# Optimization experiments

Measured on AMD Instinct MI355X. Metric: run time of the kernel, lower is better.

The kernel has to match this reference:

```python
import jax, jax.numpy as jnp
import numpy as np

DIM = 192
HEADS = 6
HD = DIM // HEADS
WS = 7
R = 128  # low-rank projected sequence length
N_FULL = 3136  # 56*56
B = 32


def setup_inputs() -> dict:
    key = jax.random.key(0)
    ks = jax.random.split(key, 9)
    s = 0.02
    return {
        "x": jax.random.normal(ks[0], (2048, WS * WS, DIM), dtype=jnp.float32),
        "qkv_w": jax.random.normal(ks[1], (3 * DIM, DIM), dtype=jnp.float32) * s,
        "qkv_b": jax.random.normal(ks[2], (3 * DIM,), dtype=jnp.float32) * s,
        "E_w": jax.random.normal(ks[3], (R, N_FULL), dtype=jnp.float32) * s,
        "E_b": jax.random.normal(ks[4], (R,), dtype=jnp.float32) * s,
        "F_w": jax.random.normal(ks[5], (R, N_FULL), dtype=jnp.float32) * s,
        "F_b": jax.random.normal(ks[6], (R,), dtype=jnp.float32) * s,
        "proj_w": jax.random.normal(ks[7], (DIM, DIM), dtype=jnp.float32) * s,
        "proj_b": jax.random.normal(ks[8], (DIM,), dtype=jnp.float32) * s,
        "h": 56,
        "w": 56,
    }


def reference(x, qkv_w, qkv_b, E_w, E_b, F_w, F_b, proj_w, proj_b, h, w):
    C = x.shape[-1]
    # window_reverse: (nW*B, ws*ws, C) -> (B, H*W, C)
    xw = x.reshape(-1, WS, WS, C)
    b = xw.shape[0] // ((h // WS) * (w // WS))
    xm = xw.reshape(b, h // WS, w // WS, WS, WS, C)
    xm = xm.transpose(0, 1, 3, 2, 4, 5).reshape(b, h * w, C)
    n = h * w
    scale = 1.0 / np.sqrt(HD)

    qkv = (xm @ qkv_w.T + qkv_b).reshape(b, n, 3, HEADS, HD)
    qkv = qkv.transpose(2, 0, 3, 1, 4)  # (3, b, heads, n, hd)
    q, k, v = qkv[0] * scale, qkv[1], qkv[2]

    # Linformer low-rank projection along sequence: (b,h,n,d) -> (b,h,R,d)
    k_low = jnp.einsum('bhnd,kn->bhkd', k, E_w) + E_b[None, None, :, None]
    v_low = jnp.einsum('bhnd,kn->bhkd', v, F_w) + F_b[None, None, :, None]

    attn = jnp.einsum('bhnd,bhkd->bhnk', q, k_low)  # (b, heads, n, R)
    attn = jax.nn.softmax(attn, axis=-1)

    out = jnp.einsum('bhnk,bhkd->bhnd', attn, v_low)
    out = out.transpose(0, 2, 1, 3).reshape(b, n, C)
    out = out @ proj_w.T + proj_b
    return out
```

## Files before the change

kernel.cpp:

```cpp
#include <hip/hip_runtime.h>

typedef __bf16 bf16;
typedef bf16 bf16x8 __attribute__((ext_vector_type(8)));
typedef bf16 bf16x4 __attribute__((ext_vector_type(4)));
typedef float f32x4 __attribute__((ext_vector_type(4)));

#define MFMA16(a,b,c) __builtin_amdgcn_mfma_f32_16x16x32_bf16(a,b,c,0,0,0)

#define NSEQ 3136
#define CDIM 192

__device__ inline bf16x8 cvt8(float4 a, float4 b) {
  bf16x8 r;
  r[0]=(bf16)a.x; r[1]=(bf16)a.y; r[2]=(bf16)a.z; r[3]=(bf16)a.w;
  r[4]=(bf16)b.x; r[5]=(bf16)b.y; r[6]=(bf16)b.z; r[7]=(bf16)b.w;
  return r;
}

__device__ inline bf16x4 cvt4(float4 a) {
  bf16x4 r;
  r[0]=(bf16)a.x; r[1]=(bf16)a.y; r[2]=(bf16)a.z; r[3]=(bf16)a.w;
  return r;
}

__global__ void k_convert(const float* __restrict__ qkv_w, const float* __restrict__ E_w,
                          const float* __restrict__ F_w, const float* __restrict__ proj_w,
                          bf16* __restrict__ qkvw, bf16* __restrict__ EF, bf16* __restrict__ projw) {
  int i4 = blockIdx.x * blockDim.x + threadIdx.x;
  const int tot4 = 950272 / 4;
  for (; i4 < tot4; i4 += gridDim.x * blockDim.x) {
    int i = i4 * 4;
    float4 f;
    bf16* dst;
    if (i < 110592)      { f = *(const float4*)(qkv_w + i);            dst = qkvw + i; }
    else if (i < 512000) { f = *(const float4*)(E_w + (i - 110592));   dst = EF + (i - 110592); }
    else if (i < 913408) { f = *(const float4*)(F_w + (i - 512000));   dst = EF + (i - 110592); }
    else                 { f = *(const float4*)(proj_w + (i - 913408)); dst = projw + (i - 913408); }
    *(bf16x4*)dst = cvt4(f);
  }
}

__global__ void k_rowsum(const float* __restrict__ E_w, const float* __restrict__ F_w,
                         float* __restrict__ rowsums) {
  __shared__ float red[4];
  int row = blockIdx.x;
  const float* src = (row < 128) ? (E_w + (long)row * NSEQ) : (F_w + (long)(row - 128) * NSEQ);
  float s = 0.f;
  for (int i = threadIdx.x; i < NSEQ; i += 256) s += src[i];
  for (int off = 32; off; off >>= 1) s += __shfl_xor(s, off);
  if ((threadIdx.x & 63) == 0) red[threadIdx.x >> 6] = s;
  __syncthreads();
  if (threadIdx.x == 0) rowsums[row] = red[0] + red[1] + red[2] + red[3];
}

__global__ void k_xT(const float* __restrict__ x, bf16* __restrict__ xmT) {
  __shared__ bf16 tile[64][196];
  int blk = blockIdx.x;
  int b = blk / 49, n0 = (blk % 49) * 64;
  int tid = threadIdx.x;
  for (int e = tid; e < 3072; e += 256) {
    int row = e / 48, c4 = e % 48;
    int n = n0 + row;
    int r = n / 56, cc = n % 56;
    long srcrow = (long)(b * 64 + (r / 7) * 8 + (cc / 7)) * 49 + (r % 7) * 7 + (cc % 7);
    float4 f = *(const float4*)(x + srcrow * 192 + c4 * 4);
    *(bf16x4*)&tile[row][c4 * 4] = cvt4(f);
  }
  __syncthreads();
  for (int e = tid; e < 1536; e += 256) {
    int c = e >> 3, k = e & 7;
    bf16x8 v;
    for (int jj = 0; jj < 8; jj++) v[jj] = tile[k * 8 + jj][c];
    *(bf16x8*)(xmT + ((long)b * 192 + c) * NSEQ + n0 + k * 8) = v;
  }
}

__launch_bounds__(256)
__global__ void k_xlow(const bf16* __restrict__ EF, const bf16* __restrict__ xmT,
                       float* __restrict__ partial) {
  __shared__ bf16 As[64][72];
  __shared__ bf16 Bs[64][72];
  int idx = blockIdx.x;
  int s = idx % 7;
  int rem = (idx / 7) % 12;
  int b = idx / 84;
  int m0 = (rem / 3) * 64, n0 = (rem % 3) * 64;
  int kbase = s * 448;
  int tid = threadIdx.x;
  int wid = tid >> 6, lane = tid & 63;
  int wm = wid >> 1, wn = wid & 1;
  int lrow = lane & 15, lk = (lane >> 4) * 8;
  int srow = tid >> 2, skoff = (tid & 3) * 16;
  const bf16* Ap = EF + (long)(m0 + srow) * NSEQ + kbase + skoff;
  const bf16* Bp = xmT + ((long)b * 192 + n0 + srow) * NSEQ + kbase + skoff;
  f32x4 zero = {0.f, 0.f, 0.f, 0.f};
  f32x4 acc[2][2];
  for (int i = 0; i < 2; i++) for (int j = 0; j < 2; j++) acc[i][j] = zero;
  for (int k0 = 0; k0 < 448; k0 += 64) {
    *(bf16x8*)&As[srow][skoff]     = *(const bf16x8*)(Ap + k0);
    *(bf16x8*)&As[srow][skoff + 8] = *(const bf16x8*)(Ap + k0 + 8);
    *(bf16x8*)&Bs[srow][skoff]     = *(const bf16x8*)(Bp + k0);
    *(bf16x8*)&Bs[srow][skoff + 8] = *(const bf16x8*)(Bp + k0 + 8);
    __syncthreads();
    for (int ks = 0; ks < 2; ks++) {
      bf16x8 af[2], bfv[2];
      for (int i = 0; i < 2; i++) af[i]  = *(bf16x8*)&As[wm * 32 + 16 * i + lrow][ks * 32 + lk];
      for (int j = 0; j < 2; j++) bfv[j] = *(bf16x8*)&Bs[wn * 32 + 16 * j + lrow][ks * 32 + lk];
      for (int i = 0; i < 2; i++) for (int j = 0; j < 2; j++) acc[i][j] = MFMA16(af[i], bfv[j], acc[i][j]);
    }
    __syncthreads();
  }
  float* P = partial + (long)idx * 4096;
  for (int i = 0; i < 2; i++) for (int j = 0; j < 2; j++) for (int rr = 0; rr < 4; rr++) {
    int rl = wm * 32 + 16 * i + (lane >> 4) * 4 + rr;
    int cl = wn * 32 + 16 * j + lrow;
    P[rl * 64 + cl] = acc[i][j][rr];
  }
}

__global__ void k_reduce(const float* __restrict__ partial, bf16* __restrict__ el_fl) {
  int idx = blockIdx.x;
  int qtr = idx & 3;
  int bt = idx >> 2;
  int t = bt % 12, b = bt / 12;
  const float* P = partial + (long)bt * 7 * 4096 + qtr * 1024;
  int tid = threadIdx.x;
  float4 sum = {0.f, 0.f, 0.f, 0.f};
  for (int s = 0; s < 7; s++) {
    float4 f = *(const float4*)(P + s * 4096 + tid * 4);
    sum.x += f.x; sum.y += f.y; sum.z += f.z; sum.w += f.w;
  }
  int ee = qtr * 1024 + tid * 4;
  int lm = ee >> 6, lc = ee & 63;
  int kr = (t / 3) * 64 + lm, c = (t % 3) * 64 + lc;
  *(bf16x4*)(el_fl + ((long)b * 256 + kr) * 192 + c) = cvt4(sum);
}

__launch_bounds__(256)
__global__ void k_lowproj(const bf16* __restrict__ el_fl, const bf16* __restrict__ qkvw,
                          const float* __restrict__ qkv_b, const float* __restrict__ E_b,
                          const float* __restrict__ F_b, const float* __restrict__ rowsums,
                          bf16* __restrict__ k_low, bf16* __restrict__ v_lowT) {
  __shared__ bf16 As[64][200];
  __shared__ bf16 Bs[64][200];
  int idx = blockIdx.x;
  int b = idx / 12, rem = idx % 12;
  int type = rem / 6; rem %= 6;
  int bm, bn;
  if (type == 0) { bm = rem / 3; bn = rem % 3; }
  else           { bm = rem / 2; bn = rem % 2; }
  int m0 = bm * 64, n0 = bn * 64;
  int tid = threadIdx.x;
  int wid = tid >> 6, lane = tid & 63;
  int wm = wid >> 1, wn = wid & 1;
  int lrow = lane & 15, lk = (lane >> 4) * 8;
  int srow = tid >> 2, skoff = (tid & 3) * 16;
  const bf16* Ap; const bf16* Bp;
  if (type == 0) {
    Ap = el_fl + ((long)b * 256 + m0 + srow) * 192 + skoff;
    Bp = qkvw + (long)(192 + n0 + srow) * 192 + skoff;
  } else {
    Ap = qkvw + (long)(384 + m0 + srow) * 192 + skoff;
    Bp = el_fl + ((long)b * 256 + 128 + n0 + srow) * 192 + skoff;
  }
  for (int kk = 0; kk < 192; kk += 64) {
    *(bf16x8*)&As[srow][kk + skoff]     = *(const bf16x8*)(Ap + kk);
    *(bf16x8*)&As[srow][kk + skoff + 8] = *(const bf16x8*)(Ap + kk + 8);
    *(bf16x8*)&Bs[srow][kk + skoff]     = *(const bf16x8*)(Bp + kk);
    *(bf16x8*)&Bs[srow][kk + skoff + 8] = *(const bf16x8*)(Bp + kk + 8);
  }
  __syncthreads();
  f32x4 zero = {0.f, 0.f, 0.f, 0.f};
  f32x4 acc[2][2];
  for (int i = 0; i < 2; i++) for (int j = 0; j < 2; j++) acc[i][j] = zero;
  for (int ks = 0; ks < 6; ks++) {
    bf16x8 af[2], bfv[2];
    for (int i = 0; i < 2; i++) af[i]  = *(bf16x8*)&As[wm * 32 + 16 * i + lrow][ks * 32 + lk];
    for (int j = 0; j < 2; j++) bfv[j] = *(bf16x8*)&Bs[wn * 32 + 16 * j + lrow][ks * 32 + lk];
    for (int i = 0; i < 2; i++) for (int j = 0; j < 2; j++) acc[i][j] = MFMA16(af[i], bfv[j], acc[i][j]);
  }
  if (type == 0) {
    for (int i = 0; i < 2; i++) for (int j = 0; j < 2; j++) for (int rr = 0; rr < 4; rr++) {
      int kr = m0 + wm * 32 + 16 * i + (lane >> 4) * 4 + rr;
      int c = n0 + wn * 32 + 16 * j + lrow;
      float v = acc[i][j][rr] + rowsums[kr] * qkv_b[192 + c] + E_b[kr];
      k_low[((long)b * 128 + kr) * 192 + c] = (bf16)v;
    }
  } else {
    for (int i = 0; i < 2; i++) for (int j = 0; j < 2; j++) for (int rr = 0; rr < 4; rr++) {
      int c = m0 + wm * 32 + 16 * i + (lane >> 4) * 4 + rr;
      int kr = n0 + wn * 32 + 16 * j + lrow;
      float v = acc[i][j][rr] + rowsums[128 + kr] * qkv_b[384 + c] + F_b[kr];
      v_lowT[((long)b * 192 + c) * 128 + kr] = (bf16)v;
    }
  }
}

__launch_bounds__(256)
__global__ void k_qgemm2(const float* __restrict__ x, const bf16* __restrict__ qkvw,
                         const float* __restrict__ qkv_b, bf16* __restrict__ q) {
  __shared__ bf16 As[128][104];
  __shared__ bf16 Bs[192][200];
  long g0 = (long)blockIdx.x * 128;
  int tid = threadIdx.x;
  int wid = tid >> 6, lane = tid & 63;
  int lrow = lane & 15, lk = (lane >> 4) * 8;
  {
    int koff = (tid & 3) * 48;
    for (int r0 = 0; r0 < 192; r0 += 64) {
      int row = r0 + (tid >> 2);
      const bf16* Bp = qkvw + (long)row * 192 + koff;
      for (int m = 0; m < 6; m++)
        *(bf16x8*)&Bs[row][koff + 8 * m] = *(const bf16x8*)(Bp + 8 * m);
    }
  }
  int arow = tid >> 1, half = tid & 1;
  long g = g0 + arow;
  int b = (int)(g / NSEQ), n = (int)(g % NSEQ);
  int r = n / 56, cc = n % 56;
  long srcrow = (long)(b * 64 + (r / 7) * 8 + (cc / 7)) * 49 + (r % 7) * 7 + (cc % 7);
  const float* Ap = x + srcrow * 192 + half * 48;
  f32x4 zero = {0.f, 0.f, 0.f, 0.f};
  f32x4 acc[2][12];
  for (int i = 0; i < 2; i++) for (int j = 0; j < 12; j++) acc[i][j] = zero;
  for (int k0 = 0; k0 < 192; k0 += 96) {
    for (int m = 0; m < 3; m++) {
      const float4* xp = (const float4*)(Ap + k0 + 16 * m);
      float4 f0 = xp[0], f1 = xp[1];
      float4 f2 = xp[2], f3 = xp[3];
      *(bf16x8*)&As[arow][half * 48 + 16 * m] = cvt8(f0, f1);
      *(bf16x8*)&As[arow][half * 48 + 16 * m + 8] = cvt8(f2, f3);
    }
    __syncthreads();
    for (int ks = 0; ks < 3; ks++) {
      bf16x8 af[2];
      for (int i = 0; i < 2; i++) af[i] = *(bf16x8*)&As[wid * 32 + 16 * i + lrow][ks * 32 + lk];
      for (int j = 0; j < 12; j++) {
        bf16x8 bv = *(bf16x8*)&Bs[16 * j + lrow][k0 + ks * 32 + lk];
        acc[0][j] = MFMA16(af[0], bv, acc[0][j]);
        acc[1][j] = MFMA16(af[1], bv, acc[1][j]);
      }
    }
    __syncthreads();
  }
  const float scale = 0.17677669529663687f;
  for (int i = 0; i < 2; i++) for (int j = 0; j < 12; j++) for (int rr = 0; rr < 4; rr++) {
    long grow = g0 + wid * 32 + 16 * i + (lane >> 4) * 4 + rr;
    int c = 16 * j + lrow;
    float v = (acc[i][j][rr] + qkv_b[c]) * scale;
    q[grow * 192 + c] = (bf16)v;
  }
}

__launch_bounds__(256)
__global__ void k_attn(const bf16* __restrict__ q, const bf16* __restrict__ k_low,
                       const bf16* __restrict__ v_lowT, bf16* __restrict__ out_att) {
  __shared__ bf16 Ks[128][40];
  __shared__ bf16 Vs[32][136];
  __shared__ bf16 Ps[4][16][136];
  int idx = blockIdx.x;
  int nt = idx % 49, bh = idx / 49;
  int h = bh % 6, b = bh / 6;
  int n0 = nt * 64;
  int tid = threadIdx.x;
  int wid = tid >> 6, lane = tid & 63;
  int lrow = lane & 15, lk = (lane >> 4) * 8;
  {
    int row = tid >> 1, koff = (tid & 1) * 16;
    const bf16* src = k_low + ((long)b * 128 + row) * 192 + h * 32 + koff;
    *(bf16x8*)&Ks[row][koff] = *(const bf16x8*)src;
    *(bf16x8*)&Ks[row][koff + 8] = *(const bf16x8*)(src + 8);
  }
  {
    int row = tid >> 3, koff = (tid & 7) * 16;
    const bf16* src = v_lowT + ((long)b * 192 + h * 32 + row) * 128 + koff;
    *(bf16x8*)&Vs[row][koff] = *(const bf16x8*)src;
    *(bf16x8*)&Vs[row][koff + 8] = *(const bf16x8*)(src + 8);
  }
  int nrow = n0 + wid * 16 + lrow;
  bf16x8 qf = *(const bf16x8*)(q + ((long)b * NSEQ + nrow) * 192 + h * 32 + lk);
  __syncthreads();
  f32x4 zero = {0.f, 0.f, 0.f, 0.f};
  f32x4 s[8];
  for (int f = 0; f < 8; f++) {
    bf16x8 kf = *(bf16x8*)&Ks[16 * f + lrow][lk];
    s[f] = MFMA16(qf, kf, zero);
  }
  for (int rr = 0; rr < 4; rr++) {
    float m = s[0][rr];
    for (int f = 1; f < 8; f++) m = fmaxf(m, s[f][rr]);
    for (int off = 1; off < 16; off <<= 1) m = fmaxf(m, __shfl_xor(m, off));
    float sum = 0.f;
    for (int f = 0; f < 8; f++) { float p = __expf(s[f][rr] - m); s[f][rr] = p; sum += p; }
    for (int off = 1; off < 16; off <<= 1) sum += __shfl_xor(sum, off);
    float inv = 1.0f / sum;
    for (int f = 0; f < 8; f++) s[f][rr] *= inv;
  }
  for (int f = 0; f < 8; f++)
    for (int rr = 0; rr < 4; rr++)
      Ps[wid][(lane >> 4) * 4 + rr][16 * f + lrow] = (bf16)s[f][rr];
  __syncthreads();
  f32x4 o[2];
  o[0] = zero; o[1] = zero;
  for (int ks = 0; ks < 4; ks++) {
    bf16x8 pf = *(bf16x8*)&Ps[wid][lrow][ks * 32 + lk];
    for (int j = 0; j < 2; j++) {
      bf16x8 vf = *(bf16x8*)&Vs[16 * j + lrow][ks * 32 + lk];
      o[j] = MFMA16(pf, vf, o[j]);
    }
  }
  for (int j = 0; j < 2; j++) for (int rr = 0; rr < 4; rr++) {
    int nn = n0 + wid * 16 + (lane >> 4) * 4 + rr;
    out_att[((long)b * NSEQ + nn) * 192 + h * 32 + 16 * j + lrow] = (bf16)o[j][rr];
  }
}

__launch_bounds__(256)
__global__ void k_proj(const bf16* __restrict__ oa, const bf16* __restrict__ projw,
                       const float* __restrict__ proj_b, float* __restrict__ out) {
  __shared__ bf16 As[128][104];
  __shared__ bf16 Bs[192][200];
  long g0 = (long)blockIdx.x * 128;
  int tid = threadIdx.x;
  int wid = tid >> 6, lane = tid & 63;
  int lrow = lane & 15, lk = (lane >> 4) * 8;
  {
    int koff = (tid & 3) * 48;
    for (int r0 = 0; r0 < 192; r0 += 64) {
      int row = r0 + (tid >> 2);
      const bf16* Bp = projw + (long)row * 192 + koff;
      for (int m = 0; m < 6; m++)
        *(bf16x8*)&Bs[row][koff + 8 * m] = *(const bf16x8*)(Bp + 8 * m);
    }
  }
  int arow = tid >> 1, half = tid & 1;
  const bf16* Ap = oa + (g0 + arow) * 192 + half * 48;
  f32x4 zero = {0.f, 0.f, 0.f, 0.f};
  f32x4 acc[2][12];
  for (int i = 0; i < 2; i++) for (int j = 0; j < 12; j++) acc[i][j] = zero;
  for (int k0 = 0; k0 < 192; k0 += 96) {
    for (int m = 0; m < 6; m++)
      *(bf16x8*)&As[arow][half * 48 + 8 * m] = *(const bf16x8*)(Ap + k0 + 8 * m);
    __syncthreads();
    for (int ks = 0; ks < 3; ks++) {
      bf16x8 af[2];
      for (int i = 0; i < 2; i++) af[i] = *(bf16x8*)&As[wid * 32 + 16 * i + lrow][ks * 32 + lk];
      for (int j = 0; j < 12; j++) {
        bf16x8 bv = *(bf16x8*)&Bs[16 * j + lrow][k0 + ks * 32 + lk];
        acc[0][j] = MFMA16(af[0], bv, acc[0][j]);
        acc[1][j] = MFMA16(af[1], bv, acc[1][j]);
      }
    }
    __syncthreads();
  }
  for (int i = 0; i < 2; i++) for (int j = 0; j < 12; j++) for (int rr = 0; rr < 4; rr++) {
    long grow = g0 + wid * 32 + 16 * i + (lane >> 4) * 4 + rr;
    int c = 16 * j + lrow;
    out[grow * 192 + c] = acc[i][j][rr] + proj_b[c];
  }
}

extern "C" void kernel_launch(void* const* d_in, const int* in_sizes, int n_in,
                              void* d_out, int out_size, void* d_ws, size_t ws_size,
                              hipStream_t stream) {
  const float* x      = (const float*)d_in[0];
  const float* qkv_w  = (const float*)d_in[1];
  const float* qkv_b  = (const float*)d_in[2];
  const float* E_w    = (const float*)d_in[3];
  const float* E_b    = (const float*)d_in[4];
  const float* F_w    = (const float*)d_in[5];
  const float* F_b    = (const float*)d_in[6];
  const float* proj_w = (const float*)d_in[7];
  const float* proj_b = (const float*)d_in[8];
  float* out = (float*)d_out;

  char* ws = (char*)d_ws;
  size_t off = 0;
  auto alloc = [&](size_t bytes) { char* p = ws + off; off += (bytes + 255) & ~(size_t)255; return p; };
  bf16* qkvw     = (bf16*)alloc((size_t)110592 * 2);
  bf16* EF       = (bf16*)alloc((size_t)802816 * 2);
  bf16* projw    = (bf16*)alloc((size_t)36864 * 2);
  float* rowsums = (float*)alloc((size_t)256 * 4);
  bf16* xmT      = (bf16*)alloc((size_t)32 * 192 * NSEQ * 2);
  float* partial = (float*)alloc((size_t)2688 * 4096 * 4);
  bf16* q        = (bf16*)partial;
  bf16* el_fl    = (bf16*)alloc((size_t)32 * 256 * 192 * 2);
  bf16* k_low    = (bf16*)alloc((size_t)32 * 128 * 192 * 2);
  bf16* v_lowT   = (bf16*)alloc((size_t)32 * 192 * 128 * 2);
  bf16* out_att  = xmT;

  k_convert<<<dim3(480), dim3(256), 0, stream>>>(qkv_w, E_w, F_w, proj_w, qkvw, EF, projw);
  k_rowsum<<<dim3(256), dim3(256), 0, stream>>>(E_w, F_w, rowsums);
  k_xT<<<dim3(32 * 49), dim3(256), 0, stream>>>(x, xmT);
  k_xlow<<<dim3(2688), dim3(256), 0, stream>>>(EF, xmT, partial);
  k_reduce<<<dim3(1536), dim3(256), 0, stream>>>(partial, el_fl);
  k_lowproj<<<dim3(384), dim3(256), 0, stream>>>(el_fl, qkvw, qkv_b, E_b, F_b, rowsums, k_low, v_lowT);
  k_qgemm2<<<dim3(784), dim3(256), 0, stream>>>(x, qkvw, qkv_b, q);
  k_attn<<<dim3(32 * 6 * 49), dim3(256), 0, stream>>>(q, k_low, v_lowT, out_att);
  k_proj<<<dim3(784), dim3(256), 0, stream>>>(out_att, projw, proj_b, out);
}
```

Measured before the change: 319.0 us.

## Retile low-rank projection GEMM to full-output blocks and streamline attention softmax

The sequence-projection GEMM now computes the full 256x192 output per batch and k-split in one 512-thread block, instead of 12 separate 64x64 tiles. This eliminates repeated loads of the projection weights and input across tiles, and the reduce kernel is adjusted to the new partial layout. The attention kernel swaps MFMA operands so each lane owns one query row, which cuts cross-lane shuffles and enables packed stores of probabilities. The row-sum kernel is vectorised. The trade-off is fewer blocks (224) than CUs and high accumulator register use.

```diff
diff --git a/kernel.cpp b/kernel.cpp
--- a/kernel.cpp
+++ b/kernel.cpp
@@ -46,7 +46,10 @@
   int row = blockIdx.x;
   const float* src = (row < 128) ? (E_w + (long)row * NSEQ) : (F_w + (long)(row - 128) * NSEQ);
   float s = 0.f;
-  for (int i = threadIdx.x; i < NSEQ; i += 256) s += src[i];
+  for (int i = threadIdx.x; i < 784; i += 256) {
+    float4 f = *(const float4*)(src + i * 4);
+    s += f.x + f.y + f.z + f.w;
+  }
   for (int off = 32; off; off >>= 1) s += __shfl_xor(s, off);
   if ((threadIdx.x & 63) == 0) red[threadIdx.x >> 6] = s;
   __syncthreads();
@@ -75,65 +78,60 @@
   }
 }
 
-__launch_bounds__(256)
+__launch_bounds__(512)
 __global__ void k_xlow(const bf16* __restrict__ EF, const bf16* __restrict__ xmT,
                        float* __restrict__ partial) {
-  __shared__ bf16 As[64][72];
-  __shared__ bf16 Bs[64][72];
+  __shared__ bf16 As[256][72];
+  __shared__ bf16 Bs[192][72];
   int idx = blockIdx.x;
-  int s = idx % 7;
-  int rem = (idx / 7) % 12;
-  int b = idx / 84;
-  int m0 = (rem / 3) * 64, n0 = (rem % 3) * 64;
+  int s = idx % 7, b = idx / 7;
   int kbase = s * 448;
   int tid = threadIdx.x;
   int wid = tid >> 6, lane = tid & 63;
-  int wm = wid >> 1, wn = wid & 1;
-  int lrow = lane & 15, lk = (lane >> 4) * 8;
-  int srow = tid >> 2, skoff = (tid & 3) * 16;
-  const bf16* Ap = EF + (long)(m0 + srow) * NSEQ + kbase + skoff;
-  const bf16* Bp = xmT + ((long)b * 192 + n0 + srow) * NSEQ + kbase + skoff;
+  int wm = wid >> 2, wn = wid & 3;
+  int lrow = lane & 15, hi = lane >> 4, lk = hi * 8;
   f32x4 zero = {0.f, 0.f, 0.f, 0.f};
-  f32x4 acc[2][2];
-  for (int i = 0; i < 2; i++) for (int j = 0; j < 2; j++) acc[i][j] = zero;
+  f32x4 acc[8][3];
+  for (int i = 0; i < 8; i++) for (int j = 0; j < 3; j++) acc[i][j] = zero;
   for (int k0 = 0; k0 < 448; k0 += 64) {
-    *(bf16x8*)&As[srow][skoff]     = *(const bf16x8*)(Ap + k0);
-    *(bf16x8*)&As[srow][skoff + 8] = *(const bf16x8*)(Ap + k0 + 8);
-    *(bf16x8*)&Bs[srow][skoff]     = *(const bf16x8*)(Bp + k0);
-    *(bf16x8*)&Bs[srow][skoff + 8] = *(const bf16x8*)(Bp + k0 + 8);
+    for (int i = 0; i < 4; i++) {
+      int unit = i * 512 + tid;
+      int row = unit >> 3, koff = (unit & 7) * 8;
+      *(bf16x8*)&As[row][koff] = *(const bf16x8*)(EF + (long)row * NSEQ + kbase + k0 + koff);
+    }
+    for (int i = 0; i < 3; i++) {
+      int unit = i * 512 + tid;
+      int row = unit >> 3, koff = (unit & 7) * 8;
+      *(bf16x8*)&Bs[row][koff] = *(const bf16x8*)(xmT + ((long)b * 192 + row) * NSEQ + kbase + k0 + koff);
+    }
     __syncthreads();
     for (int ks = 0; ks < 2; ks++) {
-      bf16x8 af[2], bfv[2];
-      for (int i = 0; i < 2; i++) af[i]  = *(bf16x8*)&As[wm * 32 + 16 * i + lrow][ks * 32 + lk];
-      for (int j = 0; j < 2; j++) bfv[j] = *(bf16x8*)&Bs[wn * 32 + 16 * j + lrow][ks * 32 + lk];
-      for (int i = 0; i < 2; i++) for (int j = 0; j < 2; j++) acc[i][j] = MFMA16(af[i], bfv[j], acc[i][j]);
-    }
-    __syncthreads();
-  }
-  float* P = partial + (long)idx * 4096;
-  for (int i = 0; i < 2; i++) for (int j = 0; j < 2; j++) for (int rr = 0; rr < 4; rr++) {
-    int rl = wm * 32 + 16 * i + (lane >> 4) * 4 + rr;
-    int cl = wn * 32 + 16 * j + lrow;
-    P[rl * 64 + cl] = acc[i][j][rr];
+      bf16x8 af[8], bfv[3];
+      for (int i = 0; i < 8; i++) af[i]  = *(bf16x8*)&As[wm * 128 + 16 * i + lrow][ks * 32 + lk];
+      for (int j = 0; j < 3; j++) bfv[j] = *(bf16x8*)&Bs[wn * 48 + 16 * j + lrow][ks * 32 + lk];
+      for (int i = 0; i < 8; i++) for (int j = 0; j < 3; j++) acc[i][j] = MFMA16(af[i], bfv[j], acc[i][j]);
+    }
+    __syncthreads();
+  }
+  float* P = partial + (long)idx * 49152;
+  for (int i = 0; i < 8; i++) for (int j = 0; j < 3; j++) for (int rr = 0; rr < 4; rr++) {
+    int rl = wm * 128 + 16 * i + hi * 4 + rr;
+    int cl = wn * 48 + 16 * j + lrow;
+    P[rl * 192 + cl] = acc[i][j][rr];
   }
 }
 
 __global__ void k_reduce(const float* __restrict__ partial, bf16* __restrict__ el_fl) {
-  int idx = blockIdx.x;
-  int qtr = idx & 3;
-  int bt = idx >> 2;
-  int t = bt % 12, b = bt / 12;
-  const float* P = partial + (long)bt * 7 * 4096 + qtr * 1024;
-  int tid = threadIdx.x;
+  int blk = blockIdx.x;
+  int b = blk / 48, ch = blk % 48;
+  long e = (long)ch * 1024 + threadIdx.x * 4;
+  const float* P = partial + (long)b * 7 * 49152 + e;
   float4 sum = {0.f, 0.f, 0.f, 0.f};
   for (int s = 0; s < 7; s++) {
-    float4 f = *(const float4*)(P + s * 4096 + tid * 4);
+    float4 f = *(const float4*)(P + (long)s * 49152);
     sum.x += f.x; sum.y += f.y; sum.z += f.z; sum.w += f.w;
   }
-  int ee = qtr * 1024 + tid * 4;
-  int lm = ee >> 6, lc = ee & 63;
-  int kr = (t / 3) * 64 + lm, c = (t % 3) * 64 + lc;
-  *(bf16x4*)(el_fl + ((long)b * 256 + kr) * 192 + c) = cvt4(sum);
+  *(bf16x4*)(el_fl + (long)b * 49152 + e) = cvt4(sum);
 }
 
 __launch_bounds__(256)
@@ -264,7 +262,7 @@
   int n0 = nt * 64;
   int tid = threadIdx.x;
   int wid = tid >> 6, lane = tid & 63;
-  int lrow = lane & 15, lk = (lane >> 4) * 8;
+  int lrow = lane & 15, hi = lane >> 4, lk = hi * 8;
   {
     int row = tid >> 1, koff = (tid & 1) * 16;
     const bf16* src = k_low + ((long)b * 128 + row) * 192 + h * 32 + koff;
@@ -284,21 +282,25 @@
   f32x4 s[8];
   for (int f = 0; f < 8; f++) {
     bf16x8 kf = *(bf16x8*)&Ks[16 * f + lrow][lk];
-    s[f] = MFMA16(qf, kf, zero);
-  }
-  for (int rr = 0; rr < 4; rr++) {
-    float m = s[0][rr];
-    for (int f = 1; f < 8; f++) m = fmaxf(m, s[f][rr]);
-    for (int off = 1; off < 16; off <<= 1) m = fmaxf(m, __shfl_xor(m, off));
-    float sum = 0.f;
-    for (int f = 0; f < 8; f++) { float p = __expf(s[f][rr] - m); s[f][rr] = p; sum += p; }
-    for (int off = 1; off < 16; off <<= 1) sum += __shfl_xor(sum, off);
-    float inv = 1.0f / sum;
-    for (int f = 0; f < 8; f++) s[f][rr] *= inv;
-  }
-  for (int f = 0; f < 8; f++)
-    for (int rr = 0; rr < 4; rr++)
-      Ps[wid][(lane >> 4) * 4 + rr][16 * f + lrow] = (bf16)s[f][rr];
+    s[f] = MFMA16(kf, qf, zero);
+  }
+  float m = s[0][0];
+  for (int f = 0; f < 8; f++) for (int rr = 0; rr < 4; rr++) m = fmaxf(m, s[f][rr]);
+  m = fmaxf(m, __shfl_xor(m, 16));
+  m = fmaxf(m, __shfl_xor(m, 32));
+  float sum = 0.f;
+  for (int f = 0; f < 8; f++) for (int rr = 0; rr < 4; rr++) {
+    float p = __expf(s[f][rr] - m);
+    s[f][rr] = p; sum += p;
+  }
+  sum += __shfl_xor(sum, 16);
+  sum += __shfl_xor(sum, 32);
+  float inv = 1.0f / sum;
+  for (int f = 0; f < 8; f++) {
+    bf16x4 pv;
+    for (int rr = 0; rr < 4; rr++) pv[rr] = (bf16)(s[f][rr] * inv);
+    *(bf16x4*)&Ps[wid][lrow][16 * f + hi * 4] = pv;
+  }
   __syncthreads();
   f32x4 o[2];
   o[0] = zero; o[1] = zero;
@@ -310,7 +312,7 @@
     }
   }
   for (int j = 0; j < 2; j++) for (int rr = 0; rr < 4; rr++) {
-    int nn = n0 + wid * 16 + (lane >> 4) * 4 + rr;
+    int nn = n0 + wid * 16 + hi * 4 + rr;
     out_att[((long)b * NSEQ + nn) * 192 + h * 32 + 16 * j + lrow] = (bf16)o[j][rr];
   }
 }
@@ -382,7 +384,7 @@
   bf16* projw    = (bf16*)alloc((size_t)36864 * 2);
   float* rowsums = (float*)alloc((size_t)256 * 4);
   bf16* xmT      = (bf16*)alloc((size_t)32 * 192 * NSEQ * 2);
-  float* partial = (float*)alloc((size_t)2688 * 4096 * 4);
+  float* partial = (float*)alloc((size_t)224 * 49152 * 4);
   bf16* q        = (bf16*)partial;
   bf16* el_fl    = (bf16*)alloc((size_t)32 * 256 * 192 * 2);
   bf16* k_low    = (bf16*)alloc((size_t)32 * 128 * 192 * 2);
@@ -392,7 +394,7 @@
   k_convert<<<dim3(480), dim3(256), 0, stream>>>(qkv_w, E_w, F_w, proj_w, qkvw, EF, projw);
   k_rowsum<<<dim3(256), dim3(256), 0, stream>>>(E_w, F_w, rowsums);
   k_xT<<<dim3(32 * 49), dim3(256), 0, stream>>>(x, xmT);
-  k_xlow<<<dim3(2688), dim3(256), 0, stream>>>(EF, xmT, partial);
+  k_xlow<<<dim3(224), dim3(512), 0, stream>>>(EF, xmT, partial);
   k_reduce<<<dim3(1536), dim3(256), 0, stream>>>(partial, el_fl);
   k_lowproj<<<dim3(384), dim3(256), 0, stream>>>(el_fl, qkvw, qkv_b, E_b, F_b, rowsums, k_low, v_lowT);
   k_qgemm2<<<dim3(784), dim3(256), 0, stream>>>(x, qkvw, qkv_b, q);
```

Measured after the change: 300.5 us. 5.8% less time.
